# Performance work log

Measured on AMD Instinct MI355X. Metric: run time of the kernel, lower is better.

The kernel has to match this reference:

```python
import jax, jax.numpy as jnp
import numpy as np

N_NODES = 50000
N_EDGES = 800000
IN_DIM = 128
HID = 128
NUM_CLASSES = 2


def setup_inputs() -> dict:
    key = jax.random.key(0)
    ks = jax.random.split(key, 16)
    inp = {
        "adj_row": jax.random.randint(ks[0], (N_EDGES,), 0, N_NODES),
        "adj_col": jax.random.randint(ks[1], (N_EDGES,), 0, N_NODES),
        "adj_vals": jax.random.uniform(ks[2], (N_EDGES,), dtype=jnp.float32),
        "input_feature": jax.random.normal(ks[3], (N_NODES, IN_DIM), dtype=jnp.float32),
        "graph_indicator": jax.random.randint(ks[4], (N_NODES,), 0, 64),
        # GCN layer params (kaiming-uniform-ish init; zeros bias like the torch module)
        "W1": jax.random.uniform(ks[5], (IN_DIM, HID), jnp.float32, -1, 1) * np.sqrt(6.0 / IN_DIM),
        "b1": jnp.zeros((HID,), jnp.float32),
        "W2": jax.random.uniform(ks[6], (HID, HID), jnp.float32, -1, 1) * np.sqrt(6.0 / HID),
        "b2": jnp.zeros((HID,), jnp.float32),
        "W3": jax.random.uniform(ks[7], (HID, HID), jnp.float32, -1, 1) * np.sqrt(6.0 / HID),
        "b3": jnp.zeros((HID,), jnp.float32),
        # fc params (torch.nn.Linear default init range)
        "fcW1": jax.random.uniform(ks[8], (3 * HID, HID), jnp.float32, -1, 1) / np.sqrt(3 * HID),
        "fcb1": jax.random.uniform(ks[9], (HID,), jnp.float32, -1, 1) / np.sqrt(3 * HID),
        "fcW2": jax.random.uniform(ks[10], (HID, HID // 2), jnp.float32, -1, 1) / np.sqrt(HID),
        "fcb2": jax.random.uniform(ks[11], (HID // 2,), jnp.float32, -1, 1) / np.sqrt(HID),
        "fcW3": jax.random.uniform(ks[12], (HID // 2, NUM_CLASSES), jnp.float32, -1, 1) / np.sqrt(HID // 2),
        "fcb3": jax.random.uniform(ks[13], (NUM_CLASSES,), jnp.float32, -1, 1) / np.sqrt(HID // 2),
    }
    return inp


def _gcn_layer(row, col, vals, x, W, b, n_nodes):
    # support = X @ W  -> dense GEMM
    support = x @ W
    # sparse.mm(A, support): out[i] = sum_{e: row[e]=i} vals[e] * support[col[e]]
    msgs = support[col] * vals[:, None]  # [E, D] gather + scale
    agg = jax.ops.segment_sum(msgs, row, num_segments=n_nodes)
    return agg + b


def reference(adj_row, adj_col, adj_vals, input_feature, graph_indicator,
              W1, b1, W2, b2, W3, b3, fcW1, fcb1, fcW2, fcb2, fcW3, fcb3):
    n = input_feature.shape[0]
    g1 = jax.nn.relu(_gcn_layer(adj_row, adj_col, adj_vals, input_feature, W1, b1, n))
    g2 = jax.nn.relu(_gcn_layer(adj_row, adj_col, adj_vals, g1, W2, b2, n))
    g3 = jax.nn.relu(_gcn_layer(adj_row, adj_col, adj_vals, g2, W3, b3, n))
    feat = jnp.concatenate([g1, g2, g3], axis=1)  # [N, 3*HID]
    h = jax.nn.relu(feat @ fcW1 + fcb1)
    h = jax.nn.relu(h @ fcW2 + fcb2)
    logits = h @ fcW3 + fcb3
    return logits
```

## Files before the change

### kernel.cpp

```cpp
#include <hip/hip_runtime.h>
#include <hip/hip_bf16.h>

#define N_NODES 50000
#define N_EDGES 800000
#define NBK 782
#define BCAP 1408
#define PADSLACK 448

static inline int cdiv(int a, int b) { return (a + b - 1) / b; }

typedef __attribute__((ext_vector_type(8))) short short8;
typedef __attribute__((ext_vector_type(4))) float f32x4;

__device__ __forceinline__ float b2f(unsigned short u) {
    union { unsigned int i; float f; } c;
    c.i = ((unsigned int)u) << 16;
    return c.f;
}
__device__ __forceinline__ unsigned short f2bb(float f) {
    __hip_bfloat16 h = __float2bfloat16(f);
    return *(unsigned short*)&h;
}

__device__ __forceinline__ void pack_one(const float* __restrict__ W,
                                         __hip_bfloat16* __restrict__ out,
                                         int K, int N, int t) {
    int lane = t & 63;
    int kc = (t >> 6) % (K / 32);
    int nt = (t >> 6) / (K / 32);
    int kbase = kc * 32 + (lane >> 4) * 8;
    int col = nt * 16 + (lane & 15);
    __hip_bfloat16* dst = out + (size_t)t * 8;
#pragma unroll
    for (int j = 0; j < 8; ++j)
        dst[j] = __float2bfloat16(W[(size_t)(kbase + j) * N + col]);
}

__global__ __launch_bounds__(256)
void binA_kernel(const int* __restrict__ row, const int* __restrict__ col,
                 const float* __restrict__ vals, int* __restrict__ bcursor,
                 int2* __restrict__ tmp, int E) {
    __shared__ int hist[NBK];
    __shared__ int base[NBK];
    const int tid = threadIdx.x;
    const int CH = 2048;
    int e0 = blockIdx.x * CH;
    for (int i = tid; i < NBK; i += 256) hist[i] = 0;
    __syncthreads();
    for (int i = tid; i < CH; i += 256) {
        int e = e0 + i;
        if (e < E) atomicAdd(&hist[row[e] >> 6], 1);
    }
    __syncthreads();
    for (int i = tid; i < NBK; i += 256) {
        int c = hist[i];
        base[i] = (c > 0) ? (i * BCAP + atomicAdd(&bcursor[i], c)) : 0;
        hist[i] = 0;
    }
    __syncthreads();
    for (int i = tid; i < CH; i += 256) {
        int e = e0 + i;
        if (e < E) {
            int r = row[e];
            int bk = r >> 6;
            int rk = atomicAdd(&hist[bk], 1);
            tmp[base[bk] + rk] = make_int2(((r & 63) << 16) | col[e],
                                           __float_as_int(vals[e]));
        }
    }
}

__global__ __launch_bounds__(256)
void stage1_kernel(const float* __restrict__ x, __hip_bfloat16* __restrict__ support,
                   int M,
                   const float* __restrict__ W1, const float* __restrict__ W2,
                   const float* __restrict__ W3, const float* __restrict__ fcW1,
                   const float* __restrict__ fcW2,
                   __hip_bfloat16* __restrict__ pW2, __hip_bfloat16* __restrict__ pW3,
                   __hip_bfloat16* __restrict__ pfcW1, __hip_bfloat16* __restrict__ pfcW2) {
    __shared__ unsigned short As[64][136];
    const int b = blockIdx.x;
    const int tid = threadIdx.x;

    if (b < 782) {
        const int wave = tid >> 6;
        const int lane = tid & 63;
        const int ln15 = lane & 15;
        const int quad = lane >> 4;
        const int m0 = b * 64;

        short8 bfr[4][2];
#pragma unroll
        for (int kc = 0; kc < 4; ++kc)
#pragma unroll
            for (int h = 0; h < 2; ++h)
#pragma unroll
                for (int j = 0; j < 8; ++j)
                    bfr[kc][h][j] = (short)f2bb(
                        W1[(size_t)(kc * 32 + quad * 8 + j) * 128 + (wave * 2 + h) * 16 + ln15]);

#pragma unroll
        for (int i = 0; i < 4; ++i) {
            int idx = tid + i * 256;
            int r = idx >> 4;
            int c8 = (idx & 15) * 8;
            uint4 pk = {0, 0, 0, 0};
            if (m0 + r < M) {
                const float* src = &x[(size_t)(m0 + r) * 128 + c8];
                float4 a = *(const float4*)src;
                float4 bq = *(const float4*)(src + 4);
                pk.x = f2bb(a.x) | ((unsigned int)f2bb(a.y) << 16);
                pk.y = f2bb(a.z) | ((unsigned int)f2bb(a.w) << 16);
                pk.z = f2bb(bq.x) | ((unsigned int)f2bb(bq.y) << 16);
                pk.w = f2bb(bq.z) | ((unsigned int)f2bb(bq.w) << 16);
            }
            *(uint4*)&As[r][c8] = pk;
        }
        __syncthreads();

        f32x4 acc[4][2];
#pragma unroll
        for (int s = 0; s < 4; ++s)
#pragma unroll
            for (int h = 0; h < 2; ++h) acc[s][h] = (f32x4){0.f, 0.f, 0.f, 0.f};
#pragma unroll
        for (int kc = 0; kc < 4; ++kc) {
            short8 af[4];
#pragma unroll
            for (int s = 0; s < 4; ++s)
                af[s] = *(const short8*)&As[s * 16 + ln15][kc * 32 + quad * 8];
#pragma unroll
            for (int s = 0; s < 4; ++s)
#pragma unroll
                for (int h = 0; h < 2; ++h)
                    acc[s][h] = __builtin_amdgcn_mfma_f32_16x16x32_bf16(
                        af[s], bfr[kc][h], acc[s][h], 0, 0, 0);
        }
#pragma unroll
        for (int s = 0; s < 4; ++s)
#pragma unroll
            for (int h = 0; h < 2; ++h) {
                int cl = (wave * 2 + h) * 16 + ln15;
#pragma unroll
                for (int r = 0; r < 4; ++r) {
                    int rw = m0 + s * 16 + quad * 4 + r;
                    if (rw < M)
                        support[(size_t)rw * 128 + cl] = __float2bfloat16(acc[s][h][r]);
                }
            }
        return;
    }

    int pb = b - 782;
    if (pb < 8)       pack_one(W2,  pW2,  128, 128, pb * 256 + tid);
    else if (pb < 16) pack_one(W3,  pW3,  128, 128, (pb - 8) * 256 + tid);
    else if (pb < 40) pack_one(fcW1, pfcW1, 384, 128, (pb - 16) * 256 + tid);
    else              pack_one(fcW2, pfcW2, 128, 64, (pb - 40) * 256 + tid);
}

__global__ __launch_bounds__(256)
void binB_kernel(const int2* __restrict__ tmp, const int* __restrict__ bcursor,
                 int2* __restrict__ rowrange, int2* __restrict__ epack, int N) {
    int b = blockIdx.x;
    int r0 = b << 6;
    int nr = N - r0; if (nr > 64) nr = 64;
    __shared__ int cnt[64];
    __shared__ int cur[64];
    __shared__ int rpos[64];
    __shared__ int red[256];
    int t = threadIdx.x;
    int partial = 0;
    for (int i = t; i < b; i += 256) partial += bcursor[i];
    red[t] = partial;
    if (t < 64) cnt[t] = 0;
    __syncthreads();
    for (int off = 128; off > 0; off >>= 1) {
        if (t < off) red[t] += red[t + off];
        __syncthreads();
    }
    int slab = b * BCAP;
    int send = slab + bcursor[b];
    for (int i = slab + t; i < send; i += 256)
        atomicAdd(&cnt[tmp[i].x >> 16], 1);
    __syncthreads();
    int rcnt = (t < 64) ? cnt[t] : 0;
    int pc = (rcnt + 7) & ~7;
    if (t < 64) cur[t] = pc;
    __syncthreads();
    for (int off = 1; off < 64; off <<= 1) {
        int u = (t >= off && t < 64) ? cur[t - off] : 0;
        __syncthreads();
        if (t < 64) cur[t] += u;
        __syncthreads();
    }
    int obase = red[0] + b * PADSLACK;
    if (t < 64) {
        int pos = obase + cur[t] - pc;
        rpos[t] = pos;
        cur[t] = pos;
        if (t < nr) rowrange[r0 + t] = make_int2(pos, pos + pc);
    }
    __syncthreads();
    for (int i = slab + t; i < send; i += 256) {
        int2 v = tmp[i];
        int rl = v.x >> 16;
        int c = v.x & 0xffff;
        int pos = atomicAdd(&cur[rl], 1);
        epack[pos] = make_int2(c, v.y);
    }
    if (t < 64) {
        int rc = rcnt;
        int pos = rpos[t];
#pragma unroll 1
        for (int i = pos + rc; i < pos + pc; ++i)
            epack[i] = make_int2(0, 0);
    }
}

__device__ __forceinline__ void accum8(float* acc, long long e, uint4 u) {
    float f = __int_as_float((int)(e >> 32));
    acc[0] += f * b2f((unsigned short)(u.x & 0xffff));
    acc[1] += f * b2f((unsigned short)(u.x >> 16));
    acc[2] += f * b2f((unsigned short)(u.y & 0xffff));
    acc[3] += f * b2f((unsigned short)(u.y >> 16));
    acc[4] += f * b2f((unsigned short)(u.z & 0xffff));
    acc[5] += f * b2f((unsigned short)(u.z >> 16));
    acc[6] += f * b2f((unsigned short)(u.w & 0xffff));
    acc[7] += f * b2f((unsigned short)(u.w >> 16));
}

__device__ __forceinline__ void agg_node(const long long* __restrict__ ep,
                                         const __hip_bfloat16* __restrict__ support,
                                         int p, int end, int g, int j, float* acc) {
#pragma unroll
    for (int k = 0; k < 8; ++k) acc[k] = 0.f;
    long long e0 = 0, e1 = 0;
    uint4 u0 = {0, 0, 0, 0}, u1 = {0, 0, 0, 0};
    bool have = false;
    if (p < end) {
        e0 = ep[p + g];
        e1 = ep[p + 4 + g];
        u0 = *(const uint4*)&support[(size_t)(unsigned int)(e0 & 0xffffffffu) * 128 + j * 8];
        u1 = *(const uint4*)&support[(size_t)(unsigned int)(e1 & 0xffffffffu) * 128 + j * 8];
        p += 8;
        have = true;
    }
    while (p < end) {
        long long f0 = ep[p + g];
        long long f1 = ep[p + 4 + g];
        uint4 w0 = *(const uint4*)&support[(size_t)(unsigned int)(f0 & 0xffffffffu) * 128 + j * 8];
        uint4 w1 = *(const uint4*)&support[(size_t)(unsigned int)(f1 & 0xffffffffu) * 128 + j * 8];
        accum8(acc, e0, u0);
        accum8(acc, e1, u1);
        e0 = f0; u0 = w0; e1 = f1; u1 = w1;
        p += 8;
    }
    if (have) {
        accum8(acc, e0, u0);
        accum8(acc, e1, u1);
    }
#pragma unroll
    for (int k = 0; k < 8; ++k) {
        acc[k] += __shfl_xor(acc[k], 16);
        acc[k] += __shfl_xor(acc[k], 32);
    }
}

__device__ __forceinline__ uint4 pack_row8(const float* acc, float4 b0, float4 b1) {
    unsigned int q0 = (unsigned int)f2bb(fmaxf(acc[0] + b0.x, 0.f))
                    | ((unsigned int)f2bb(fmaxf(acc[1] + b0.y, 0.f)) << 16);
    unsigned int q1 = (unsigned int)f2bb(fmaxf(acc[2] + b0.z, 0.f))
                    | ((unsigned int)f2bb(fmaxf(acc[3] + b0.w, 0.f)) << 16);
    unsigned int q2 = (unsigned int)f2bb(fmaxf(acc[4] + b1.x, 0.f))
                    | ((unsigned int)f2bb(fmaxf(acc[5] + b1.y, 0.f)) << 16);
    unsigned int q3 = (unsigned int)f2bb(fmaxf(acc[6] + b1.z, 0.f))
                    | ((unsigned int)f2bb(fmaxf(acc[7] + b1.w, 0.f)) << 16);
    return (uint4){q0, q1, q2, q3};
}

__global__ __launch_bounds__(256, 8)
void spmm_gemm_kernel(const int2* __restrict__ rowrange,
                      const int2* __restrict__ epack,
                      const __hip_bfloat16* __restrict__ support,
                      const float* __restrict__ bias,
                      __hip_bfloat16* __restrict__ gout,
                      const __hip_bfloat16* __restrict__ pW,
                      __hip_bfloat16* __restrict__ Cout,
                      int N) {
    __shared__ unsigned short As[16][136];
    const int tid = threadIdx.x;
    const int wv = tid >> 6;
    const int l = tid & 63;
    const int g = l >> 4;
    const int j = l & 15;
    const int m0 = blockIdx.x * 16;
    const long long* ep = (const long long*)epack;
    float4 b0 = *(const float4*)&bias[j * 8];
    float4 b1 = *(const float4*)&bias[j * 8 + 4];

    for (int i = 0; i < 4; ++i) {
        int node = m0 + wv * 4 + i;
        int2 rr = rowrange[node];
        float acc[8];
        agg_node(ep, support, rr.x, rr.y, g, j, acc);
        if (g == 0) {
            uint4 st = pack_row8(acc, b0, b1);
            *(uint4*)&As[wv * 4 + i][j * 8] = st;
            *(uint4*)&gout[(size_t)node * 128 + j * 8] = st;
        }
    }
    __syncthreads();

    const int ln15 = l & 15;
    const int quad = l >> 4;
    f32x4 acc2[2];
    acc2[0] = (f32x4){0.f, 0.f, 0.f, 0.f};
    acc2[1] = (f32x4){0.f, 0.f, 0.f, 0.f};
#pragma unroll
    for (int kc = 0; kc < 4; ++kc) {
        short8 af = *(const short8*)&As[ln15][kc * 32 + quad * 8];
#pragma unroll
        for (int h = 0; h < 2; ++h) {
            int nt = wv * 2 + h;
            short8 bf = *(const short8*)&pW[((size_t)(nt * 4 + kc) * 64 + l) * 8];
            acc2[h] = __builtin_amdgcn_mfma_f32_16x16x32_bf16(af, bf, acc2[h], 0, 0, 0);
        }
    }
#pragma unroll
    for (int h = 0; h < 2; ++h) {
        int cl = (wv * 2 + h) * 16 + ln15;
#pragma unroll
        for (int r = 0; r < 4; ++r) {
            int rw = m0 + quad * 4 + r;
            Cout[(size_t)rw * 128 + cl] = __float2bfloat16(acc2[h][r]);
        }
    }
}

__global__ __launch_bounds__(256, 8)
void spmm_fc_kernel(const int2* __restrict__ rowrange,
                    const int2* __restrict__ epack,
                    const __hip_bfloat16* __restrict__ support,
                    const float* __restrict__ bias,
                    const __hip_bfloat16* __restrict__ g1,
                    const __hip_bfloat16* __restrict__ g2,
                    const __hip_bfloat16* __restrict__ pfcW1,
                    const float* __restrict__ fcb1,
                    const __hip_bfloat16* __restrict__ pfcW2,
                    const float* __restrict__ fcb2,
                    const float* __restrict__ fcW3, const float* __restrict__ fcb3,
                    float* __restrict__ out, int N) {
    __shared__ unsigned short As[16][136];
    __shared__ float w3s[128];
    __shared__ float b3s[2];
    const int tid = threadIdx.x;
    const int wv = tid >> 6;
    const int l = tid & 63;
    const int g = l >> 4;
    const int j = l & 15;
    const int m0 = blockIdx.x * 16;
    const long long* ep = (const long long*)epack;
    if (tid < 128) w3s[tid] = fcW3[tid];
    if (tid < 2) b3s[tid] = fcb3[tid];
    float4 b0 = *(const float4*)&bias[j * 8];
    float4 b1 = *(const float4*)&bias[j * 8 + 4];

    for (int i = 0; i < 4; ++i) {
        int node = m0 + wv * 4 + i;
        int2 rr = rowrange[node];
        float acc[8];
        agg_node(ep, support, rr.x, rr.y, g, j, acc);
        if (g == 0)
            *(uint4*)&As[wv * 4 + i][j * 8] = pack_row8(acc, b0, b1);
    }
    __syncthreads();

    const int ln15 = l & 15;
    const int quad = l >> 4;
    f32x4 acc[2];
    acc[0] = (f32x4){0.f, 0.f, 0.f, 0.f};
    acc[1] = (f32x4){0.f, 0.f, 0.f, 0.f};
#pragma unroll
    for (int step = 0; step < 3; ++step) {
        const int kb = (step == 0) ? 2 : (step - 1);
        if (step != 0) {
            __syncthreads();
            const __hip_bfloat16* gkb = (kb == 0) ? g1 : g2;
            int r = tid >> 4;
            int c8 = (tid & 15) * 8;
            *(uint4*)&As[r][c8] = *(const uint4*)&gkb[(size_t)(m0 + r) * 128 + c8];
            __syncthreads();
        }
#pragma unroll
        for (int kc = 0; kc < 4; ++kc) {
            short8 af = *(const short8*)&As[ln15][kc * 32 + quad * 8];
            int kcg = kb * 4 + kc;
#pragma unroll
            for (int h = 0; h < 2; ++h) {
                int nt = wv * 2 + h;
                short8 bf = *(const short8*)&pfcW1[((size_t)(nt * 12 + kcg) * 64 + l) * 8];
                acc[h] = __builtin_amdgcn_mfma_f32_16x16x32_bf16(af, bf, acc[h], 0, 0, 0);
            }
        }
    }
    __syncthreads();
#pragma unroll
    for (int h = 0; h < 2; ++h) {
        int col = (wv * 2 + h) * 16 + ln15;
        float bv = fcb1[col];
#pragma unroll
        for (int r = 0; r < 4; ++r)
            As[quad * 4 + r][col] = f2bb(fmaxf(acc[h][r] + bv, 0.f));
    }
    __syncthreads();

    f32x4 acc2 = (f32x4){0.f, 0.f, 0.f, 0.f};
#pragma unroll
    for (int kc = 0; kc < 4; ++kc) {
        short8 af = *(const short8*)&As[ln15][kc * 32 + quad * 8];
        short8 bfw = *(const short8*)&pfcW2[((size_t)(wv * 4 + kc) * 64 + l) * 8];
        acc2 = __builtin_amdgcn_mfma_f32_16x16x32_bf16(af, bfw, acc2, 0, 0, 0);
    }
    __syncthreads();
    {
        int col2 = wv * 16 + ln15;
        float bv = fcb2[col2];
#pragma unroll
        for (int r = 0; r < 4; ++r)
            As[quad * 4 + r][col2] = f2bb(fmaxf(acc2[r] + bv, 0.f));
    }
    __syncthreads();

    if (tid < 32) {
        int row = tid >> 1, cls = tid & 1;
        int grow = m0 + row;
        if (grow < N) {
            float a = b3s[cls];
#pragma unroll
            for (int k = 0; k < 64; ++k)
                a += b2f(As[row][k]) * w3s[k * 2 + cls];
            out[(size_t)grow * 2 + cls] = a;
        }
    }
}

extern "C" void kernel_launch(void* const* d_in, const int* in_sizes, int n_in,
                              void* d_out, int out_size, void* d_ws, size_t ws_size,
                              hipStream_t stream) {
    const int*   adj_row  = (const int*)d_in[0];
    const int*   adj_col  = (const int*)d_in[1];
    const float* adj_vals = (const float*)d_in[2];
    const float* x        = (const float*)d_in[3];
    const float* W1   = (const float*)d_in[5];
    const float* b1   = (const float*)d_in[6];
    const float* W2   = (const float*)d_in[7];
    const float* b2   = (const float*)d_in[8];
    const float* W3   = (const float*)d_in[9];
    const float* b3   = (const float*)d_in[10];
    const float* fcW1 = (const float*)d_in[11];
    const float* fcb1 = (const float*)d_in[12];
    const float* fcW2 = (const float*)d_in[13];
    const float* fcb2 = (const float*)d_in[14];
    const float* fcW3 = (const float*)d_in[15];
    const float* fcb3 = (const float*)d_in[16];
    float* out = (float*)d_out;

    const int N = N_NODES, E = N_EDGES;
    const int Mpad = 50048;
    const int EPAD = E + NBK * PADSLACK + 64;

    char* p = (char*)d_ws;
    auto alloc = [&](size_t bytes) {
        char* q = p;
        p += (bytes + 255) & ~(size_t)255;
        return q;
    };
    __hip_bfloat16* g1       = (__hip_bfloat16*)alloc((size_t)Mpad * 128 * 2);
    __hip_bfloat16* g2       = (__hip_bfloat16*)alloc((size_t)Mpad * 128 * 2);
    __hip_bfloat16* supportb = (__hip_bfloat16*)alloc((size_t)Mpad * 128 * 2);
    __hip_bfloat16* supportc = (__hip_bfloat16*)alloc((size_t)Mpad * 128 * 2);
    __hip_bfloat16* pW2   = (__hip_bfloat16*)alloc(16384 * 2);
    __hip_bfloat16* pW3   = (__hip_bfloat16*)alloc(16384 * 2);
    __hip_bfloat16* pfcW1 = (__hip_bfloat16*)alloc(49152 * 2);
    __hip_bfloat16* pfcW2 = (__hip_bfloat16*)alloc(8192 * 2);
    int2*  rowrange  = (int2*)alloc((size_t)(N + 1) * 8);
    int*   bcursor   = (int*)alloc((size_t)NBK * 4);
    int2*  epack     = (int2*)alloc((size_t)EPAD * 8);
    int2*  tmp       = (int2*)alloc((size_t)NBK * BCAP * 8);

    hipMemsetAsync(bcursor, 0, (size_t)NBK * 4, stream);
    binA_kernel<<<cdiv(E, 2048), 256, 0, stream>>>(adj_row, adj_col, adj_vals,
                                                   bcursor, tmp, E);
    stage1_kernel<<<826, 256, 0, stream>>>(x, supportb, N,
                                           W1, W2, W3, fcW1, fcW2,
                                           pW2, pW3, pfcW1, pfcW2);
    binB_kernel<<<NBK, 256, 0, stream>>>(tmp, bcursor, rowrange, epack, N);

    const int fgrid = cdiv(N, 16);

    spmm_gemm_kernel<<<fgrid, 256, 0, stream>>>(rowrange, epack, supportb, b1,
                                                g1, pW2, supportc, N);
    spmm_gemm_kernel<<<fgrid, 256, 0, stream>>>(rowrange, epack, supportc, b2,
                                                g2, pW3, supportb, N);
    spmm_fc_kernel<<<fgrid, 256, 0, stream>>>(rowrange, epack, supportb, b3,
                                              g1, g2, pfcW1, fcb1, pfcW2, fcb2,
                                              fcW3, fcb3, out, N);
}
```

Before: 252.3 us.

## Balance node aggregation via shared-memory work queue, add nontemporal memory ops

Replaces the fixed assignment of four nodes per wavefront with a per-block atomic counter, so wavefronts take nodes dynamically and degree imbalance inside a block evens out. Edge-list loads, gout stores and g1/g2 reloads are switched to nontemporal loads and stores to reduce cache pollution from streaming data. The final 64x2 classifier layer is spread across all 256 threads with shuffle reductions instead of 32 threads. The queue costs one shared atomic per node, and the grow<N guard is dropped in the final store.

```diff
diff --git a/kernel.cpp b/kernel.cpp
--- a/kernel.cpp
+++ b/kernel.cpp
@@ -20,6 +20,19 @@
 __device__ __forceinline__ unsigned short f2bb(float f) {
     __hip_bfloat16 h = __float2bfloat16(f);
     return *(unsigned short*)&h;
+}
+
+__device__ __forceinline__ uint4 ntload16(const void* p) {
+    union { uint4 v; unsigned long long q[2]; } r;
+    r.q[0] = __builtin_nontemporal_load((const unsigned long long*)p);
+    r.q[1] = __builtin_nontemporal_load(((const unsigned long long*)p) + 1);
+    return r.v;
+}
+__device__ __forceinline__ void ntstore16(void* p, uint4 v) {
+    union { uint4 v; unsigned long long q[2]; } r;
+    r.v = v;
+    __builtin_nontemporal_store(r.q[0], (unsigned long long*)p);
+    __builtin_nontemporal_store(r.q[1], ((unsigned long long*)p) + 1);
 }
 
 __device__ __forceinline__ void pack_one(const float* __restrict__ W,
@@ -238,16 +251,16 @@
     uint4 u0 = {0, 0, 0, 0}, u1 = {0, 0, 0, 0};
     bool have = false;
     if (p < end) {
-        e0 = ep[p + g];
-        e1 = ep[p + 4 + g];
+        e0 = __builtin_nontemporal_load(&ep[p + g]);
+        e1 = __builtin_nontemporal_load(&ep[p + 4 + g]);
         u0 = *(const uint4*)&support[(size_t)(unsigned int)(e0 & 0xffffffffu) * 128 + j * 8];
         u1 = *(const uint4*)&support[(size_t)(unsigned int)(e1 & 0xffffffffu) * 128 + j * 8];
         p += 8;
         have = true;
     }
     while (p < end) {
-        long long f0 = ep[p + g];
-        long long f1 = ep[p + 4 + g];
+        long long f0 = __builtin_nontemporal_load(&ep[p + g]);
+        long long f1 = __builtin_nontemporal_load(&ep[p + 4 + g]);
         uint4 w0 = *(const uint4*)&support[(size_t)(unsigned int)(f0 & 0xffffffffu) * 128 + j * 8];
         uint4 w1 = *(const uint4*)&support[(size_t)(unsigned int)(f1 & 0xffffffffu) * 128 + j * 8];
         accum8(acc, e0, u0);
@@ -288,6 +301,7 @@
                       __hip_bfloat16* __restrict__ Cout,
                       int N) {
     __shared__ unsigned short As[16][136];
+    __shared__ int nq;
     const int tid = threadIdx.x;
     const int wv = tid >> 6;
     const int l = tid & 63;
@@ -297,16 +311,22 @@
     const long long* ep = (const long long*)epack;
     float4 b0 = *(const float4*)&bias[j * 8];
     float4 b1 = *(const float4*)&bias[j * 8 + 4];
-
-    for (int i = 0; i < 4; ++i) {
-        int node = m0 + wv * 4 + i;
+    if (tid == 0) nq = 0;
+    __syncthreads();
+
+    for (;;) {
+        int i0 = 0;
+        if (l == 0) i0 = atomicAdd(&nq, 1);
+        i0 = __shfl(i0, 0);
+        if (i0 >= 16) break;
+        int node = m0 + i0;
         int2 rr = rowrange[node];
         float acc[8];
         agg_node(ep, support, rr.x, rr.y, g, j, acc);
         if (g == 0) {
             uint4 st = pack_row8(acc, b0, b1);
-            *(uint4*)&As[wv * 4 + i][j * 8] = st;
-            *(uint4*)&gout[(size_t)node * 128 + j * 8] = st;
+            *(uint4*)&As[i0][j * 8] = st;
+            ntstore16(&gout[(size_t)node * 128 + j * 8], st);
         }
     }
     __syncthreads();
@@ -353,6 +373,7 @@
     __shared__ unsigned short As[16][136];
     __shared__ float w3s[128];
     __shared__ float b3s[2];
+    __shared__ int nq;
     const int tid = threadIdx.x;
     const int wv = tid >> 6;
     const int l = tid & 63;
@@ -362,16 +383,22 @@
     const long long* ep = (const long long*)epack;
     if (tid < 128) w3s[tid] = fcW3[tid];
     if (tid < 2) b3s[tid] = fcb3[tid];
+    if (tid == 0) nq = 0;
     float4 b0 = *(const float4*)&bias[j * 8];
     float4 b1 = *(const float4*)&bias[j * 8 + 4];
-
-    for (int i = 0; i < 4; ++i) {
-        int node = m0 + wv * 4 + i;
+    __syncthreads();
+
+    for (;;) {
+        int i0 = 0;
+        if (l == 0) i0 = atomicAdd(&nq, 1);
+        i0 = __shfl(i0, 0);
+        if (i0 >= 16) break;
+        int node = m0 + i0;
         int2 rr = rowrange[node];
         float acc[8];
         agg_node(ep, support, rr.x, rr.y, g, j, acc);
         if (g == 0)
-            *(uint4*)&As[wv * 4 + i][j * 8] = pack_row8(acc, b0, b1);
+            *(uint4*)&As[i0][j * 8] = pack_row8(acc, b0, b1);
     }
     __syncthreads();
 
@@ -388,7 +415,7 @@
             const __hip_bfloat16* gkb = (kb == 0) ? g1 : g2;
             int r = tid >> 4;
             int c8 = (tid & 15) * 8;
-            *(uint4*)&As[r][c8] = *(const uint4*)&gkb[(size_t)(m0 + r) * 128 + c8];
+            *(uint4*)&As[r][c8] = ntload16(&gkb[(size_t)(m0 + r) * 128 + c8]);
             __syncthreads();
         }
 #pragma unroll
@@ -431,15 +458,20 @@
     }
     __syncthreads();
 
-    if (tid < 32) {
-        int row = tid >> 1, cls = tid & 1;
-        int grow = m0 + row;
-        if (grow < N) {
-            float a = b3s[cls];
-#pragma unroll
-            for (int k = 0; k < 64; ++k)
-                a += b2f(As[row][k]) * w3s[k * 2 + cls];
-            out[(size_t)grow * 2 + cls] = a;
+    {
+        int oidx = tid >> 3;
+        int s = tid & 7;
+        int row = oidx >> 1, cls = oidx & 1;
+        float a = 0.f;
+#pragma unroll
+        for (int k = s * 8; k < s * 8 + 8; ++k)
+            a += b2f(As[row][k]) * w3s[k * 2 + cls];
+        a += __shfl_xor(a, 1);
+        a += __shfl_xor(a, 2);
+        a += __shfl_xor(a, 4);
+        if (s == 0) {
+            int grow = m0 + row;
+            __builtin_nontemporal_store(a + b3s[cls], &out[(size_t)grow * 2 + cls]);
         }
     }
 }
```

Result: slower. 273.3 us (+8.3%).
